# Kernel optimization log

Hardware: AMD Instinct MI355X
Metric: run time of the kernel (lower is better)

Reference implementation:

```python
import jax, jax.numpy as jnp
import numpy as np


def _knn_hypergraph_G(feat, k=5, m_prob=1.0):
    # feat: [N, D] node features. Returns G = Dv^-1/2 H De^-1 H^T Dv^-1/2 (HGNN utils).
    N = feat.shape[0]
    sq = jnp.sum(feat * feat, axis=1)
    d2 = sq[:, None] + sq[None, :] - 2.0 * (feat @ feat.T)
    d = jnp.sqrt(jnp.maximum(d2, 0.0))
    d = jnp.maximum(d, d.T)
    d = d * (1.0 - jnp.eye(N, dtype=feat.dtype))  # zero diagonal (self distance)
    avg = jnp.mean(d, axis=1)                      # per-center average distance
    _, nn_idx = jax.lax.top_k(-d, k)               # k nearest per center (incl. self)
    dn = jnp.take_along_axis(d, nn_idx, axis=1)    # [N, k]
    w = jnp.exp(-(dn ** 2) / (m_prob * avg[:, None]) ** 2)
    H = jnp.zeros((N, N), feat.dtype)
    centers = jnp.arange(N)[:, None]
    H = H.at[nn_idx, centers].set(w)               # H[node, hyperedge=center]
    DV = H.sum(axis=1)
    DE = H.sum(axis=0)
    Hn = H * (1.0 / DE)[None, :]
    dvi = DV ** -0.5
    return dvi[:, None] * (Hn @ H.T) * dvi[None, :]


def setup_inputs():
    key = jax.random.key(0)
    ks = jax.random.split(key, 16)
    B = 8
    def g(i, shape, scale=0.02):
        return jax.random.normal(ks[i], shape, dtype=jnp.float32) * scale
    return {
        "x": jax.random.normal(ks[0], (B, 3, 448, 448), dtype=jnp.float32),
        "x_f": jax.random.normal(ks[1], (B, 36), dtype=jnp.float32),
        "conv1_w": g(2, (64, 3, 5, 5)), "conv1_b": jnp.zeros((64,), jnp.float32),
        "conv2_w": g(3, (32, 64, 5, 5)), "conv2_b": jnp.zeros((32,), jnp.float32),
        "enc_w": g(4, (36, 512)), "enc_b": jnp.zeros((512,), jnp.float32),
        "wq": g(5, (512, 512)), "bq": jnp.zeros((512,), jnp.float32),
        "wk": g(6, (512, 512)), "bk": jnp.zeros((512,), jnp.float32),
        "wv": g(7, (512, 512)), "bv": jnp.zeros((512,), jnp.float32),
        "wo": g(8, (512, 512)), "bo": jnp.zeros((512,), jnp.float32),
        "dec_w": g(9, (512, 32)), "dec_b": jnp.zeros((32,), jnp.float32),
        "hg_w1": g(10, (2500, 512)), "hg_b1": jnp.zeros((512,), jnp.float32),
        "hg_w2": g(11, (512, 32)), "hg_b2": jnp.zeros((32,), jnp.float32),
        "head_w": g(12, (32, 1000)), "head_b": jnp.zeros((1000,), jnp.float32),
    }


def reference(x, x_f, conv1_w, conv1_b, conv2_w, conv2_b, enc_w, enc_b,
              wq, bq, wk, bk, wv, bv, wo, bo, dec_w, dec_b,
              hg_w1, hg_b1, hg_w2, hg_b2, head_w, head_b):
    B = x.shape[0]
    # fusion_model is undefined upstream; identity channel-reorder fusion.
    xi = jnp.concatenate([x[:, 2:3], x[:, 1:2], x[:, 0:1]], axis=1)  # [B,3,448,448]

    def conv(h, w, b):
        y = jax.lax.conv_general_dilated(h, w, (3, 3), [(2, 2), (2, 2)],
                                         dimension_numbers=("NCHW", "OIHW", "NCHW"))
        return y + b[None, :, None, None]

    h = jax.nn.relu(conv(xi, conv1_w, conv1_b))  # [B,64,150,150]
    h = jax.nn.relu(conv(h, conv2_w, conv2_b))   # [B,32,50,50]

    # feature branch: 36 -> 512 -> self-attention (2 heads of 256, batch as tokens) -> 32
    f = jax.nn.relu(x_f @ enc_w + enc_b)         # [B,512]
    nh, hd = 2, 256
    q = (f @ wq + bq).reshape(B, nh, hd).transpose(1, 0, 2)
    kk = (f @ wk + bk).reshape(B, nh, hd).transpose(1, 0, 2)
    v = (f @ wv + bv).reshape(B, nh, hd).transpose(1, 0, 2)
    attn = jax.nn.softmax(jnp.einsum("hbd,hcd->hbc", q, kk) / jnp.sqrt(jnp.float32(hd)), axis=-1)
    f = jnp.einsum("hbc,hcd->hbd", attn, v).transpose(1, 0, 2).reshape(B, nh * hd)
    f = f @ wo + bo
    f = jax.nn.relu(f @ dec_w + dec_b)           # [B,32]

    # hypergraph branch: per-sample KNN hyperedges over 32 channel-nodes (dim 2500)
    ft = h.reshape(B, 32, 50 * 50)

    def per_sample(fti):
        G = _knn_hypergraph_G(fti)                       # [32,32]
        z = jax.nn.relu(G @ (fti @ hg_w1 + hg_b1))       # HGNN layer 1 (2500->512)
        return G @ (z @ hg_w2 + hg_b2)                   # HGNN layer 2 (512->32)

    g = jax.vmap(per_sample)(ft)                         # [B,32,32]
    out = g.mean(axis=1) + f                             # [B,32]
    logits = out @ head_w + head_b                       # [B,1000]
    return (logits, f)
```

## Files before the change

### kernel.cpp

```cpp
#include <hip/hip_runtime.h>
#include <hip/hip_bf16.h>

#define RFL(x) __builtin_amdgcn_readfirstlane(x)

__global__ void __launch_bounds__(256) wT_k(const float* __restrict__ c1w,
                                            const float* __restrict__ c2w,
                                            float* __restrict__ c1wT,
                                            float* __restrict__ c2wT) {
  int idx = blockIdx.x * 256 + threadIdx.x;
  if (idx < 4800) {
    int o = idx / 75, k = idx % 75;
    c1wT[k * 64 + o] = c1w[idx];
  } else if (idx < 56000) {
    int j = idx - 4800;
    int o = j / 1600, k = j % 1600;
    c2wT[k * 32 + o] = c2w[j];
  }
}

__global__ void __launch_bounds__(512) conv1_k(const float* __restrict__ x,
                                               const float* __restrict__ wT,
                                               const float* __restrict__ bias,
                                               float* __restrict__ out) {
  __shared__ float xt[3][8][456];
  int b = blockIdx.x / 75;
  int py2 = blockIdx.x % 75;
  int t = threadIdx.x;
  int iy0 = py2 * 6 - 2;
  if (t < 456) {
    int ix = t - 2;
    bool cok = (ix >= 0) && (ix < 448);
#pragma unroll
    for (int c = 0; c < 3; ++c) {
      const float* xp = x + (size_t)(b * 3 + (2 - c)) * 200704;
#pragma unroll
      for (int r = 0; r < 8; ++r) {
        int iy = iy0 + r;
        bool rok = (iy >= 0) && (iy < 448);
        xt[c][r][t] = (rok && cok) ? xp[(size_t)iy * 448 + ix] : 0.f;
      }
    }
  }
  __syncthreads();
  int lane = t & 63;
  int w = RFL(t >> 6);
  int pl = w >> 2;
  int ob = (w & 3) * 16;
  int py = py2 * 2 + pl;
  int rbase = pl * 3;
  for (int sub = 0; sub < 3; ++sub) {
    int px = sub * 64 + lane;
    int pxc = min(px, 149);
    float acc[16];
#pragma unroll
    for (int u = 0; u < 16; ++u) acc[u] = 0.f;
    for (int c = 0; c < 3; ++c)
#pragma unroll
      for (int ky = 0; ky < 5; ++ky)
#pragma unroll
        for (int kx = 0; kx < 5; ++kx) {
          float xv = xt[c][rbase + ky][pxc * 3 + kx];
          const float* wr = wT + (c * 25 + ky * 5 + kx) * 64 + ob;
#pragma unroll
          for (int u = 0; u < 16; ++u) acc[u] += xv * wr[u];
        }
    if (px < 150) {
#pragma unroll
      for (int u = 0; u < 16; ++u)
        out[(size_t)(b * 64 + ob + u) * 22500 + py * 150 + px] =
            fmaxf(acc[u] + bias[ob + u], 0.f);
    }
  }
}

__global__ void __launch_bounds__(512) conv2p_k(const float* __restrict__ h1,
                                                const float* __restrict__ wT,
                                                float* __restrict__ part2) {
  __shared__ float ht[8][8][152];
  int blk = blockIdx.x;
  int ch = blk & 7;
  int bpy = blk >> 3;
  int b = bpy / 25;
  int py2 = bpy % 25;
  int t = threadIdx.x;
  int iy0 = py2 * 6 - 2;
  const float* hbase = h1 + (size_t)(b * 64 + ch * 8) * 22500;
  {
    int sub = t >> 7;
    int col = t & 127;
    bool cok = col >= 2;
#pragma unroll
    for (int i = 0; i < 16; ++i) {
      int c = sub * 2 + (i >> 3);
      const int r = i & 7;
      int iy = iy0 + r;
      bool ok = (iy >= 0) & (iy < 150) & cok;
      float v = ok ? hbase[c * 22500 + iy * 150 + (col - 2)] : 0.f;
      ht[c][r][col] = v;
    }
#pragma unroll
    for (int it = 0; it < 3; ++it) {
      int e = it * 512 + t;
      int pair = (e * 2731) >> 16;
      int col2 = e - pair * 24;
      int c = pair >> 3, r = pair & 7;
      int iy = iy0 + r;
      bool ok = (iy >= 0) & (iy < 150);
      float v = ok ? hbase[c * 22500 + iy * 150 + 126 + col2] : 0.f;
      ht[c][r][128 + col2] = v;
    }
  }
  __syncthreads();
  int lane = t & 63;
  int w = RFL(t >> 6);
  int pl = w >> 2;
  int ob = (w & 3) * 8;
  int py = py2 * 2 + pl;
  int rbase = pl * 3;
  int pxc = min(lane, 49);
  float acc[8];
#pragma unroll
  for (int u = 0; u < 8; ++u) acc[u] = 0.f;
#pragma unroll
  for (int c = 0; c < 8; ++c)
#pragma unroll
    for (int ky = 0; ky < 5; ++ky)
#pragma unroll
      for (int kx = 0; kx < 5; ++kx) {
        float xv = ht[c][rbase + ky][pxc * 3 + kx];
        const float* wr = wT + ((ch * 8 + c) * 25 + ky * 5 + kx) * 32 + ob;
#pragma unroll
        for (int u = 0; u < 8; ++u) acc[u] += xv * wr[u];
      }
  if (lane < 50) {
#pragma unroll
    for (int u = 0; u < 8; ++u)
      part2[((size_t)ch * 256 + b * 32 + ob + u) * 2500 + py * 50 + lane] = acc[u];
  }
}

__global__ void __launch_bounds__(256) comb2g_k(const float* __restrict__ part2,
                                                const float* __restrict__ bias,
                                                float* __restrict__ ft,
                                                float* __restrict__ gramP) {
  __shared__ float tile[32][102];
  __shared__ float tileT[100][36];
  int b = blockIdx.x, pc = blockIdx.y;
  int p0 = pc * 100;
  int t = threadIdx.x;
  for (int e = t; e < 3200; e += 256) {
    int o = e / 100, p = e % 100;
    float s = bias[o];
#pragma unroll
    for (int ch = 0; ch < 8; ++ch)
      s += part2[((size_t)ch * 256 + b * 32 + o) * 2500 + p0 + p];
    float v = fmaxf(s, 0.f);
    tile[o][p] = v;
    tileT[p][o] = v;
  }
  __syncthreads();
  for (int e = t; e < 3200; e += 256) {
    int o = e / 100, p = e % 100;
    ft[(size_t)(b * 32 + o) * 2500 + p0 + p] = tile[o][p];
  }
  int i = t >> 3, j0 = (t & 7) * 4;
  float4 a = make_float4(0.f, 0.f, 0.f, 0.f);
  for (int p = 0; p < 100; ++p) {
    float ai = tileT[p][i];
    float4 bj = *(const float4*)&tileT[p][j0];
    a.x += ai * bj.x; a.y += ai * bj.y; a.z += ai * bj.z; a.w += ai * bj.w;
  }
  *(float4*)(gramP + ((size_t)(b * 25 + pc)) * 1024 + t * 4) = a;
}

__global__ void __launch_bounds__(256) conv2_fb_k(const float* __restrict__ h1,
                                                  const float* __restrict__ w,
                                                  const float* __restrict__ bias,
                                                  float* __restrict__ ft,
                                                  float* __restrict__ ftT) {
  __shared__ float ht[16][5][152];
  __shared__ float tile[32][51];
  int b = blockIdx.x / 50;
  int py = blockIdx.x % 50;
  int t = threadIdx.x;
  int lane = t & 63;
  int ob = RFL(t >> 6) * 8;
  int px = lane;
  int pxc = min(px, 49);
  int iy0 = py * 3 - 2;
  float acc[8];
#pragma unroll
  for (int u = 0; u < 8; ++u) acc[u] = 0.f;
  for (int ch = 0; ch < 4; ++ch) {
    __syncthreads();
    for (int e = t; e < 12160; e += 256) {
      int c = e / 760;
      int rest = e % 760;
      int r = rest / 152;
      int col = rest % 152;
      int iy = iy0 + r;
      int ix = col - 2;
      float v = 0.f;
      if (iy >= 0 && iy < 150 && ix >= 0 && ix < 150)
        v = h1[((size_t)(b * 64 + ch * 16 + c) * 150 + iy) * 150 + ix];
      ht[c][r][col] = v;
    }
    __syncthreads();
    for (int c = 0; c < 16; ++c) {
#pragma unroll
      for (int ky = 0; ky < 5; ++ky)
#pragma unroll
        for (int kx = 0; kx < 5; ++kx) {
          float xv = ht[c][ky][pxc * 3 + kx];
#pragma unroll
          for (int u = 0; u < 8; ++u)
            acc[u] += xv * w[(ob + u) * 1600 + (ch * 16 + c) * 25 + ky * 5 + kx];
        }
    }
  }
  if (px < 50) {
#pragma unroll
    for (int u = 0; u < 8; ++u)
      tile[ob + u][px] = fmaxf(acc[u] + bias[ob + u], 0.f);
  }
  __syncthreads();
  for (int e = t; e < 1600; e += 256) {
    int o = e / 50, p = e % 50;
    ft[(size_t)(b * 32 + o) * 2500 + py * 50 + p] = tile[o][p];
  }
  for (int e = t; e < 1600; e += 256) {
    int p = e >> 5, o = e & 31;
    ftT[((size_t)b * 2500 + py * 50 + p) * 32 + o] = tile[o][p];
  }
}

__global__ void __launch_bounds__(256) hg_gram_fb_k(const float* __restrict__ ftT,
                                                    float* __restrict__ gramP) {
  __shared__ float sl[100][32];
  int b = blockIdx.x, ch = blockIdx.y;
  const float* S = ftT + (size_t)b * 80000 + ch * 3200;
  int t = threadIdx.x;
  for (int e = t; e < 800; e += 256)
    ((float4*)sl)[e] = ((const float4*)S)[e];
  __syncthreads();
  int i = t >> 3, j0 = (t & 7) * 4;
  float4 a = make_float4(0.f, 0.f, 0.f, 0.f);
  for (int p = 0; p < 100; ++p) {
    float ai = sl[p][i];
    float4 bj = *(const float4*)&sl[p][j0];
    a.x += ai * bj.x; a.y += ai * bj.y; a.z += ai * bj.z; a.w += ai * bj.w;
  }
  *(float4*)(gramP + ((size_t)(b * 25 + ch)) * 1024 + t * 4) = a;
}

__global__ void __launch_bounds__(512) fk_enc(const float* __restrict__ xf,
                                              const float* __restrict__ ew,
                                              const float* __restrict__ eb,
                                              float* __restrict__ f) {
  int b = blockIdx.x, j = threadIdx.x;
  float acc = eb[j];
  for (int c = 0; c < 36; ++c) acc += xf[b * 36 + c] * ew[c * 512 + j];
  f[b * 512 + j] = fmaxf(acc, 0.f);
}

__global__ void __launch_bounds__(512) fk_qkv(const float* __restrict__ f,
                                              const float* __restrict__ wq, const float* __restrict__ bq,
                                              const float* __restrict__ wk, const float* __restrict__ bk,
                                              const float* __restrict__ wv, const float* __restrict__ bv,
                                              float* __restrict__ qkv) {
  __shared__ float fs[512];
  int b = blockIdx.x, m = blockIdx.y, j = threadIdx.x;
  const float* W = (m == 0) ? wq : (m == 1) ? wk : wv;
  const float* B = (m == 0) ? bq : (m == 1) ? bk : bv;
  fs[j] = f[b * 512 + j];
  __syncthreads();
  float acc = B[j];
  for (int c = 0; c < 512; ++c) acc += fs[c] * W[(size_t)c * 512 + j];
  qkv[(m * 8 + b) * 512 + j] = acc;
}

__global__ void __launch_bounds__(512) fk_ao_k(const float* __restrict__ qkv,
                                               const float* __restrict__ wo, const float* __restrict__ bo,
                                               const float* __restrict__ dw, const float* __restrict__ db,
                                               float* __restrict__ f2) {
  __shared__ float att[2][8];
  __shared__ float aos[512];
  __shared__ float os[512];
  int b = blockIdx.x, t = threadIdx.x;
  const float* q = qkv;
  const float* kk = qkv + 4096;
  const float* v = qkv + 8192;
  {
    int g = t >> 5, l = t & 31;
    int h = g >> 3, c = g & 7;
    const float* qb = q + b * 512 + h * 256;
    const float* kc = kk + c * 512 + h * 256;
    float s = 0.f;
    for (int d = l; d < 256; d += 32) s += qb[d] * kc[d];
#pragma unroll
    for (int m = 16; m >= 1; m >>= 1) s += __shfl_xor(s, m);
    if (l == 0) att[h][c] = s * (1.f / 16.f);
  }
  __syncthreads();
  if (t < 2) {
    int h = t;
    float mx = -1e30f;
#pragma unroll
    for (int c = 0; c < 8; ++c) mx = fmaxf(mx, att[h][c]);
    float e[8], s = 0.f;
#pragma unroll
    for (int c = 0; c < 8; ++c) { e[c] = expf(att[h][c] - mx); s += e[c]; }
#pragma unroll
    for (int c = 0; c < 8; ++c) att[h][c] = e[c] / s;
  }
  __syncthreads();
  {
    int j = t, h = j >> 8;
    float acc = 0.f;
#pragma unroll
    for (int c = 0; c < 8; ++c) acc += att[h][c] * v[c * 512 + j];
    aos[j] = acc;
  }
  __syncthreads();
  {
    int j = t;
    float acc = bo[j];
    for (int c = 0; c < 512; ++c) acc += aos[c] * wo[(size_t)c * 512 + j];
    os[j] = acc;
  }
  __syncthreads();
  if (t < 32) {
    float a2 = db[t];
    for (int c = 0; c < 512; ++c) a2 += os[c] * dw[c * 32 + t];
    f2[b * 32 + t] = fmaxf(a2, 0.f);
  }
}

__global__ void __launch_bounds__(256) hg_G2_k(const float* __restrict__ gramP,
                                               float* __restrict__ Gout) {
  int b = blockIdx.x;
  __shared__ float gram[32][32];
  __shared__ float d[32][32];
  __shared__ float avg[32];
  __shared__ float Hm[32][32];
  __shared__ float Hn[32][32];
  __shared__ float DE[32];
  __shared__ float dvi[32];
  int t = threadIdx.x;
  {
    float4 s = make_float4(0.f, 0.f, 0.f, 0.f);
    for (int ch = 0; ch < 25; ++ch) {
      float4 v = *(const float4*)(gramP + ((size_t)(b * 25 + ch)) * 1024 + t * 4);
      s.x += v.x; s.y += v.y; s.z += v.z; s.w += v.w;
    }
    *(float4*)(&gram[0][0] + t * 4) = s;
  }
  __syncthreads();
  for (int e = t; e < 1024; e += 256) {
    int i = e >> 5, j = e & 31;
    float d2 = gram[i][i] + gram[j][j] - 2.f * gram[i][j];
    float dd = sqrtf(fmaxf(d2, 0.f));
    if (i == j) dd = 0.f;
    d[i][j] = dd;
  }
  __syncthreads();
  if (t < 32) {
    float s = 0.f;
    for (int j = 0; j < 32; ++j) s += d[t][j];
    avg[t] = s * (1.f / 32.f);
  }
  for (int e = t; e < 1024; e += 256) Hm[e >> 5][e & 31] = 0.f;
  __syncthreads();
  if (t < 32) {
    unsigned picked = 0;
    float a = avg[t];
    float inv = 1.f / (a * a);
    for (int s = 0; s < 5; ++s) {
      float best = 1e30f;
      int bi = 0;
      for (int j = 0; j < 32; ++j) {
        if (picked & (1u << j)) continue;
        float dv = d[t][j];
        if (dv < best) { best = dv; bi = j; }
      }
      picked |= 1u << bi;
      Hm[bi][t] = expf(-best * best * inv);
    }
  }
  __syncthreads();
  if (t < 32) {
    float se = 0.f, sv = 0.f;
    for (int r = 0; r < 32; ++r) se += Hm[r][t];
    for (int c = 0; c < 32; ++c) sv += Hm[t][c];
    DE[t] = se;
    dvi[t] = 1.f / sqrtf(sv);
  }
  __syncthreads();
  for (int e = t; e < 1024; e += 256) {
    int i = e >> 5, j = e & 31;
    Hn[i][j] = Hm[i][j] * (1.f / DE[j]);
  }
  __syncthreads();
  for (int e = t; e < 1024; e += 256) {
    int i = e >> 5, j = e & 31;
    float acc = 0.f;
#pragma unroll
    for (int c = 0; c < 32; ++c) acc += Hn[i][c] * Hm[j][c];
    Gout[(size_t)b * 1024 + e] = dvi[i] * acc * dvi[j];
  }
}

__global__ void __launch_bounds__(512) hg_mm1_k(const float* __restrict__ ft,
                                                const float* __restrict__ w1,
                                                float* __restrict__ part) {
  int rg = blockIdx.x;
  int ch = blockIdx.y;
  int j = threadIdx.x;
  int r0 = rg * 4;
  int c0 = ch * 156 + min(ch, 4);
  int cn = 156 + (ch < 4 ? 1 : 0);
  float acc[4];
#pragma unroll
  for (int r = 0; r < 4; ++r) acc[r] = 0.f;
#pragma unroll 4
  for (int c = c0; c < c0 + cn; ++c) {
    float wv = w1[(size_t)c * 512 + j];
#pragma unroll
    for (int r = 0; r < 4; ++r)
      acc[r] += ft[(size_t)(r0 + r) * 2500 + c] * wv;
  }
#pragma unroll
  for (int r = 0; r < 4; ++r)
    part[(size_t)ch * 131072 + (r0 + r) * 512 + j] = acc[r];
}

__global__ void __launch_bounds__(256) mm1_comb_k(const float* __restrict__ part,
                                                  const float* __restrict__ b1,
                                                  float* __restrict__ t1) {
  int idx = blockIdx.x * 256 + threadIdx.x;
  if (idx >= 131072) return;
  float s = b1[idx & 511];
#pragma unroll
  for (int ch = 0; ch < 16; ++ch) s += part[(size_t)ch * 131072 + idx];
  t1[idx] = s;
}

__global__ void __launch_bounds__(512) tailz_k(const float* __restrict__ G,
                                               const float* __restrict__ t1,
                                               const float* __restrict__ w2,
                                               const float* __restrict__ b2,
                                               float* __restrict__ t2g) {
  int b = blockIdx.x, qd = blockIdx.y;
  int i0 = qd * 8;
  __shared__ float zs[8][512];
  int t = threadIdx.x;
  const float* Gb = G + b * 1024;
  const float* t1b = t1 + b * 16384;
  {
    int j = t;
    float acc[8];
#pragma unroll
    for (int i = 0; i < 8; ++i) acc[i] = 0.f;
    for (int c = 0; c < 32; ++c) {
      float tv = t1b[c * 512 + j];
#pragma unroll
      for (int i = 0; i < 8; ++i) acc[i] += Gb[(i0 + i) * 32 + c] * tv;
    }
#pragma unroll
    for (int i = 0; i < 8; ++i) zs[i][j] = fmaxf(acc[i], 0.f);
  }
  __syncthreads();
  if (t < 256) {
    int i = t >> 5, jj = t & 31;
    float acc = b2[jj];
    for (int c = 0; c < 512; ++c) acc += zs[i][c] * w2[c * 32 + jj];
    t2g[b * 1024 + (i0 + i) * 32 + jj] = acc;
  }
}

__global__ void __launch_bounds__(256) head2_k(const float* __restrict__ G,
                                               const float* __restrict__ t2g,
                                               const float* __restrict__ f2,
                                               const float* __restrict__ hw,
                                               const float* __restrict__ hb,
                                               float* __restrict__ dout) {
  int b = blockIdx.x, t = threadIdx.x;
  __shared__ float t2s[32][32];
  __shared__ float gcol[32];
  __shared__ float ov[32];
  for (int e = t; e < 1024; e += 256)
    ((float*)t2s)[e] = t2g[b * 1024 + e];
  if (t < 32) {
    float s = 0.f;
    for (int i = 0; i < 32; ++i) s += G[b * 1024 + i * 32 + t];
    gcol[t] = s;
  }
  __syncthreads();
  if (t < 32) {
    int j = t;
    float s = 0.f;
#pragma unroll
    for (int c = 0; c < 32; ++c) s += gcol[c] * t2s[c][j];
    float fv = f2[b * 32 + j];
    ov[j] = s * (1.f / 32.f) + fv;
    dout[8000 + b * 32 + j] = fv;
  }
  __syncthreads();
  for (int j = t; j < 1000; j += 256) {
    float a = hb[j];
#pragma unroll
    for (int c = 0; c < 32; ++c) a += ov[c] * hw[c * 1000 + j];
    dout[b * 1000 + j] = a;
  }
}

extern "C" void kernel_launch(void* const* d_in, const int* in_sizes, int n_in,
                              void* d_out, int out_size, void* d_ws, size_t ws_size,
                              hipStream_t stream) {
  const float* x     = (const float*)d_in[0];
  const float* xf    = (const float*)d_in[1];
  const float* c1w   = (const float*)d_in[2];
  const float* c1b   = (const float*)d_in[3];
  const float* c2w   = (const float*)d_in[4];
  const float* c2b   = (const float*)d_in[5];
  const float* enc_w = (const float*)d_in[6];
  const float* enc_b = (const float*)d_in[7];
  const float* wq    = (const float*)d_in[8];
  const float* bq    = (const float*)d_in[9];
  const float* wk    = (const float*)d_in[10];
  const float* bk    = (const float*)d_in[11];
  const float* wv    = (const float*)d_in[12];
  const float* bv    = (const float*)d_in[13];
  const float* wo    = (const float*)d_in[14];
  const float* bo    = (const float*)d_in[15];
  const float* dec_w = (const float*)d_in[16];
  const float* dec_b = (const float*)d_in[17];
  const float* w1    = (const float*)d_in[18];
  const float* b1    = (const float*)d_in[19];
  const float* w2    = (const float*)d_in[20];
  const float* b2    = (const float*)d_in[21];
  const float* hw    = (const float*)d_in[22];
  const float* hb    = (const float*)d_in[23];
  float* out = (float*)d_out;

  float* ws = (float*)d_ws;
  float* h1   = ws;
  float* ftb  = ws + 11520000;
  float* ftT  = ws + 12160000;
  float* qkv  = ws + 12800000;
  float* f    = ws + 12812288;
  float* f2   = ws + 12816384;
  float* G    = ws + 12816896;
  float* part2= ws + 12825088;
  float* c1wT = ws + 11520000;
  float* c2wT = ws + 11524800;
  float* part = ws;
  float* t1   = ws + 2097152;
  float* gramP= ws + 2228224;
  float* t2g  = ws + 2433024;

  bool big = ws_size >= (size_t)17945088 * 4;

  wT_k<<<219, 256, 0, stream>>>(c1w, c2w, c1wT, c2wT);
  conv1_k<<<8 * 75, 512, 0, stream>>>(x, c1wT, c1b, h1);
  if (big) {
    conv2p_k<<<8 * 25 * 8, 512, 0, stream>>>(h1, c2wT, part2);
    dim3 gc(8, 25);
    comb2g_k<<<gc, 256, 0, stream>>>(part2, c2b, ftb, gramP);
  } else {
    conv2_fb_k<<<8 * 50, 256, 0, stream>>>(h1, c2w, c2b, ftb, ftT);
    dim3 gg(8, 25);
    hg_gram_fb_k<<<gg, 256, 0, stream>>>(ftT, gramP);
  }

  fk_enc<<<8, 512, 0, stream>>>(xf, enc_w, enc_b, f);
  dim3 gq(8, 3);
  fk_qkv<<<gq, 512, 0, stream>>>(f, wq, bq, wk, bk, wv, bv, qkv);
  fk_ao_k<<<8, 512, 0, stream>>>(qkv, wo, bo, dec_w, dec_b, f2);

  hg_G2_k<<<8, 256, 0, stream>>>(gramP, G);
  dim3 gm(64, 16);
  hg_mm1_k<<<gm, 512, 0, stream>>>(ftb, w1, part);
  mm1_comb_k<<<512, 256, 0, stream>>>(part, b1, t1);
  dim3 gz(8, 4);
  tailz_k<<<gz, 512, 0, stream>>>(G, t1, w2, b2, t2g);
  head2_k<<<8, 256, 0, stream>>>(G, t2g, f2, hw, hb, out);
}
```

Baseline: 222.1 us.

## Split gram partials finer and restructure attention branch kernels for parallelism

The gram-partial kernels now process 50-pixel chunks over a 50-block grid instead of 100-pixel chunks over 25 blocks. comb2g now writes ft directly rather than staging it through a shared tile. In the feature branch, the encoder is fused into the qkv kernel, and the serial per-batch wo and dec stages are split into separate kernels with more blocks. The aim is to raise parallelism in small latency-bound kernels, at the cost of recomputing the encoder three times and adding one extra launch.

```diff
diff --git a/kernel.cpp b/kernel.cpp
--- a/kernel.cpp
+++ b/kernel.cpp
@@ -143,34 +143,29 @@
                                                 const float* __restrict__ bias,
                                                 float* __restrict__ ft,
                                                 float* __restrict__ gramP) {
-  __shared__ float tile[32][102];
-  __shared__ float tileT[100][36];
+  __shared__ float tileT[50][36];
   int b = blockIdx.x, pc = blockIdx.y;
-  int p0 = pc * 100;
-  int t = threadIdx.x;
-  for (int e = t; e < 3200; e += 256) {
-    int o = e / 100, p = e % 100;
+  int p0 = pc * 50;
+  int t = threadIdx.x;
+  for (int e = t; e < 1600; e += 256) {
+    int o = e / 50, p = e - o * 50;
     float s = bias[o];
 #pragma unroll
     for (int ch = 0; ch < 8; ++ch)
       s += part2[((size_t)ch * 256 + b * 32 + o) * 2500 + p0 + p];
     float v = fmaxf(s, 0.f);
-    tile[o][p] = v;
+    ft[(size_t)(b * 32 + o) * 2500 + p0 + p] = v;
     tileT[p][o] = v;
   }
   __syncthreads();
-  for (int e = t; e < 3200; e += 256) {
-    int o = e / 100, p = e % 100;
-    ft[(size_t)(b * 32 + o) * 2500 + p0 + p] = tile[o][p];
-  }
   int i = t >> 3, j0 = (t & 7) * 4;
   float4 a = make_float4(0.f, 0.f, 0.f, 0.f);
-  for (int p = 0; p < 100; ++p) {
+  for (int p = 0; p < 50; ++p) {
     float ai = tileT[p][i];
     float4 bj = *(const float4*)&tileT[p][j0];
     a.x += ai * bj.x; a.y += ai * bj.y; a.z += ai * bj.z; a.w += ai * bj.w;
   }
-  *(float4*)(gramP + ((size_t)(b * 25 + pc)) * 1024 + t * 4) = a;
+  *(float4*)(gramP + ((size_t)(b * 50 + pc)) * 1024 + t * 4) = a;
 }
 
 __global__ void __launch_bounds__(256) conv2_fb_k(const float* __restrict__ h1,
@@ -236,34 +231,25 @@
 
 __global__ void __launch_bounds__(256) hg_gram_fb_k(const float* __restrict__ ftT,
                                                     float* __restrict__ gramP) {
-  __shared__ float sl[100][32];
+  __shared__ float sl[50][32];
   int b = blockIdx.x, ch = blockIdx.y;
-  const float* S = ftT + (size_t)b * 80000 + ch * 3200;
-  int t = threadIdx.x;
-  for (int e = t; e < 800; e += 256)
+  const float* S = ftT + (size_t)b * 80000 + ch * 1600;
+  int t = threadIdx.x;
+  for (int e = t; e < 400; e += 256)
     ((float4*)sl)[e] = ((const float4*)S)[e];
   __syncthreads();
   int i = t >> 3, j0 = (t & 7) * 4;
   float4 a = make_float4(0.f, 0.f, 0.f, 0.f);
-  for (int p = 0; p < 100; ++p) {
+  for (int p = 0; p < 50; ++p) {
     float ai = sl[p][i];
     float4 bj = *(const float4*)&sl[p][j0];
     a.x += ai * bj.x; a.y += ai * bj.y; a.z += ai * bj.z; a.w += ai * bj.w;
   }
-  *(float4*)(gramP + ((size_t)(b * 25 + ch)) * 1024 + t * 4) = a;
-}
-
-__global__ void __launch_bounds__(512) fk_enc(const float* __restrict__ xf,
-                                              const float* __restrict__ ew,
-                                              const float* __restrict__ eb,
-                                              float* __restrict__ f) {
-  int b = blockIdx.x, j = threadIdx.x;
-  float acc = eb[j];
-  for (int c = 0; c < 36; ++c) acc += xf[b * 36 + c] * ew[c * 512 + j];
-  f[b * 512 + j] = fmaxf(acc, 0.f);
-}
-
-__global__ void __launch_bounds__(512) fk_qkv(const float* __restrict__ f,
+  *(float4*)(gramP + ((size_t)(b * 50 + ch)) * 1024 + t * 4) = a;
+}
+
+__global__ void __launch_bounds__(512) fk_qkv(const float* __restrict__ xf,
+                                              const float* __restrict__ ew, const float* __restrict__ eb,
                                               const float* __restrict__ wq, const float* __restrict__ bq,
                                               const float* __restrict__ wk, const float* __restrict__ bk,
                                               const float* __restrict__ wv, const float* __restrict__ bv,
@@ -272,20 +258,18 @@
   int b = blockIdx.x, m = blockIdx.y, j = threadIdx.x;
   const float* W = (m == 0) ? wq : (m == 1) ? wk : wv;
   const float* B = (m == 0) ? bq : (m == 1) ? bk : bv;
-  fs[j] = f[b * 512 + j];
+  float fe = eb[j];
+  for (int c = 0; c < 36; ++c) fe += xf[b * 36 + c] * ew[c * 512 + j];
+  fs[j] = fmaxf(fe, 0.f);
   __syncthreads();
   float acc = B[j];
   for (int c = 0; c < 512; ++c) acc += fs[c] * W[(size_t)c * 512 + j];
   qkv[(m * 8 + b) * 512 + j] = acc;
 }
 
-__global__ void __launch_bounds__(512) fk_ao_k(const float* __restrict__ qkv,
-                                               const float* __restrict__ wo, const float* __restrict__ bo,
-                                               const float* __restrict__ dw, const float* __restrict__ db,
-                                               float* __restrict__ f2) {
+__global__ void __launch_bounds__(512) fk_att(const float* __restrict__ qkv,
+                                              float* __restrict__ aog) {
   __shared__ float att[2][8];
-  __shared__ float aos[512];
-  __shared__ float os[512];
   int b = blockIdx.x, t = threadIdx.x;
   const float* q = qkv;
   const float* kk = qkv + 4096;
@@ -319,21 +303,34 @@
     float acc = 0.f;
 #pragma unroll
     for (int c = 0; c < 8; ++c) acc += att[h][c] * v[c * 512 + j];
-    aos[j] = acc;
-  }
-  __syncthreads();
-  {
-    int j = t;
-    float acc = bo[j];
-    for (int c = 0; c < 512; ++c) acc += aos[c] * wo[(size_t)c * 512 + j];
-    os[j] = acc;
-  }
-  __syncthreads();
-  if (t < 32) {
-    float a2 = db[t];
-    for (int c = 0; c < 512; ++c) a2 += os[c] * dw[c * 32 + t];
-    f2[b * 32 + t] = fmaxf(a2, 0.f);
-  }
+    aog[b * 512 + j] = acc;
+  }
+}
+
+__global__ void __launch_bounds__(256) fk_wo(const float* __restrict__ aog,
+                                             const float* __restrict__ wo,
+                                             const float* __restrict__ bo,
+                                             float* __restrict__ osg) {
+  __shared__ float aos[512];
+  int b = blockIdx.x, half = blockIdx.y, t = threadIdx.x;
+  aos[t] = aog[b * 512 + t];
+  aos[t + 256] = aog[b * 512 + t + 256];
+  __syncthreads();
+  int j = half * 256 + t;
+  float acc = bo[j];
+  for (int c = 0; c < 512; ++c) acc += aos[c] * wo[(size_t)c * 512 + j];
+  osg[b * 512 + j] = acc;
+}
+
+__global__ void __launch_bounds__(256) fk_dec(const float* __restrict__ osg,
+                                              const float* __restrict__ dw,
+                                              const float* __restrict__ db,
+                                              float* __restrict__ f2) {
+  int t = threadIdx.x;
+  int b = t >> 5, j = t & 31;
+  float acc = db[j];
+  for (int c = 0; c < 512; ++c) acc += osg[b * 512 + c] * dw[c * 32 + j];
+  f2[t] = fmaxf(acc, 0.f);
 }
 
 __global__ void __launch_bounds__(256) hg_G2_k(const float* __restrict__ gramP,
@@ -349,8 +346,8 @@
   int t = threadIdx.x;
   {
     float4 s = make_float4(0.f, 0.f, 0.f, 0.f);
-    for (int ch = 0; ch < 25; ++ch) {
-      float4 v = *(const float4*)(gramP + ((size_t)(b * 25 + ch)) * 1024 + t * 4);
+    for (int ch = 0; ch < 50; ++ch) {
+      float4 v = *(const float4*)(gramP + ((size_t)(b * 50 + ch)) * 1024 + t * 4);
       s.x += v.x; s.y += v.y; s.z += v.z; s.w += v.w;
     }
     *(float4*)(&gram[0][0] + t * 4) = s;
@@ -548,35 +545,38 @@
   float* ftb  = ws + 11520000;
   float* ftT  = ws + 12160000;
   float* qkv  = ws + 12800000;
-  float* f    = ws + 12812288;
+  float* aog  = ws + 12812288;
   float* f2   = ws + 12816384;
-  float* G    = ws + 12816896;
-  float* part2= ws + 12825088;
+  float* osg  = ws + 12816640;
+  float* G    = ws + 12820736;
+  float* part2= ws + 12828928;
   float* c1wT = ws + 11520000;
   float* c2wT = ws + 11524800;
   float* part = ws;
   float* t1   = ws + 2097152;
   float* gramP= ws + 2228224;
-  float* t2g  = ws + 2433024;
-
-  bool big = ws_size >= (size_t)17945088 * 4;
+  float* t2g  = ws + 2637824;
+
+  bool big = ws_size >= (size_t)17948928 * 4;
 
   wT_k<<<219, 256, 0, stream>>>(c1w, c2w, c1wT, c2wT);
   conv1_k<<<8 * 75, 512, 0, stream>>>(x, c1wT, c1b, h1);
   if (big) {
     conv2p_k<<<8 * 25 * 8, 512, 0, stream>>>(h1, c2wT, part2);
-    dim3 gc(8, 25);
+    dim3 gc(8, 50);
     comb2g_k<<<gc, 256, 0, stream>>>(part2, c2b, ftb, gramP);
   } else {
     conv2_fb_k<<<8 * 50, 256, 0, stream>>>(h1, c2w, c2b, ftb, ftT);
-    dim3 gg(8, 25);
+    dim3 gg(8, 50);
     hg_gram_fb_k<<<gg, 256, 0, stream>>>(ftT, gramP);
   }
 
-  fk_enc<<<8, 512, 0, stream>>>(xf, enc_w, enc_b, f);
   dim3 gq(8, 3);
-  fk_qkv<<<gq, 512, 0, stream>>>(f, wq, bq, wk, bk, wv, bv, qkv);
-  fk_ao_k<<<8, 512, 0, stream>>>(qkv, wo, bo, dec_w, dec_b, f2);
+  fk_qkv<<<gq, 512, 0, stream>>>(xf, enc_w, enc_b, wq, bq, wk, bk, wv, bv, qkv);
+  fk_att<<<8, 512, 0, stream>>>(qkv, aog);
+  dim3 gw(8, 2);
+  fk_wo<<<gw, 256, 0, stream>>>(aog, wo, bo, osg);
+  fk_dec<<<1, 256, 0, stream>>>(osg, dec_w, dec_b, f2);
 
   hg_G2_k<<<8, 256, 0, stream>>>(gramP, G);
   dim3 gm(64, 16);
```

Result: slower. 231.0 us (+4.0%).
